# Optimization experiments

Measured on AMD Instinct MI355X. Metric: run time of the kernel, lower is better.

## Reference

```python
import jax, jax.numpy as jnp
import numpy as np

R = 40000      # aug_num_rels
E = 500000     # number of relation-graph triplets
DIN = 64       # rel_emb_dim
DH = 64        # hid_dim_rel
H = 8          # num_head
DHID = DH // H # 8
NBIN = 10
L = 2          # num_layer_rel


def _leaky(x):
    return jax.nn.leaky_relu(x, negative_slope=0.2)


def _rel_layer(emb_rel, head, tail, binidx, pw, pb, abin, avec, aw, ab):
    # emb_rel: [R, DH]; head/tail/binidx: [E]
    concat = jnp.concatenate([emb_rel[head], emb_rel[tail]], axis=-1)  # [E, 2*DH]
    z = _leaky(concat @ pw + pb).reshape(-1, H, DHID)                   # [E, H, DHID]
    # attention logits: per-head dot with attn_vec + leaky(bin bias)
    raw = (z * avec[None]).sum(-1) + _leaky(abin[binidx, :, 0])         # [E, H]
    # segmented softmax over edges grouped by head index
    m = jax.ops.segment_max(raw, head, num_segments=R)                  # [R, H]
    e = jnp.exp(raw - m[head])                                          # [E, H]
    s = jax.ops.segment_sum(e, head, num_segments=R)                    # [R, H]
    beta = e / (s[head] + 1e-16)                                        # [E, H]
    msg = (emb_rel[tail] @ aw + ab).reshape(-1, H, DHID) * beta[..., None]
    out = jax.ops.segment_sum(msg, head, num_segments=R)                # [R, H, DHID]
    return out.reshape(R, DH)


def setup_inputs() -> dict:
    key = jax.random.key(0)
    ks = jax.random.split(key, 12)
    ht = jax.random.randint(ks[0], (E, 2), 0, R)
    b = jax.random.randint(ks[1], (E, 1), 0, NBIN)
    relation_triplets = jnp.concatenate([ht, b], axis=-1).astype(jnp.int64)
    sc = 0.05
    return {
        "relation_triplets": relation_triplets,
        "rel_emb_w": jax.random.normal(ks[2], (R, DIN), jnp.float32) * sc,
        "proj1_w": jax.random.normal(ks[3], (DIN, DH), jnp.float32) * sc,
        "proj1_b": jnp.zeros((DH,), jnp.float32),
        "attn_proj_w": jax.random.normal(ks[4], (L, 2 * DH, DH), jnp.float32) * sc,
        "attn_proj_b": jnp.zeros((L, DH), jnp.float32),
        "attn_bin": jax.random.normal(ks[5], (L, NBIN, H, 1), jnp.float32) * sc,
        "attn_vec": jax.random.normal(ks[6], (L, H, DHID), jnp.float32) * sc,
        "aggr_w": jax.random.normal(ks[7], (L, DH, DH), jnp.float32) * sc,
        "aggr_b": jnp.zeros((L, DH), jnp.float32),
        "res_w": jax.random.normal(ks[8], (L, DH, DH), jnp.float32) * sc,
        "res_b": jnp.zeros((L, DH), jnp.float32),
    }


def reference(relation_triplets, rel_emb_w, proj1_w, proj1_b, attn_proj_w,
              attn_proj_b, attn_bin, attn_vec, aggr_w, aggr_b, res_w, res_b):
    head = relation_triplets[:, 0]
    tail = relation_triplets[:, 1]
    binidx = relation_triplets[:, 2]
    emb_rel = jax.nn.relu(rel_emb_w @ proj1_w + proj1_b)  # [R, DH]
    for l in range(L):
        h = _rel_layer(emb_rel, head, tail, binidx,
                       attn_proj_w[l], attn_proj_b[l], attn_bin[l],
                       attn_vec[l], aggr_w[l], aggr_b[l])
        h = jax.nn.relu(h)
        emb_rel = h + jax.nn.relu(emb_rel @ res_w[l] + res_b[l])
    return emb_rel
```

## Files before the change

kernel.cpp:

```cpp
#include <hip/hip_runtime.h>
#include <hip/hip_bf16.h>

typedef __hip_bfloat16 bf16;

#define R_NUM 40000
#define E_NUM 500000

#define W_P1W 0
#define W_P1B 4096
#define W_APW 4160
#define W_APB 20544
#define W_ABIN 20672
#define W_AVEC 20832
#define W_AW 20960
#define W_AB 29152
#define W_RW 29280
#define W_RB 37472
#define W_END 37600
#define WCONV_BLOCKS 147

#define O_FLAG 0
#define O_WBUF 256
#define O_ROWP 150784
#define O_CNTS 310784
#define O_TMP 470784
#define O_PART 634624
#define O_STB 635136
#define O_BIG 2635392
#define XMP_BYTES 10240000ull
#define HR_BYTES 20480000ull
#define XM32_BYTES 20480000ull
#define NEED_LEAN (O_BIG + XMP_BYTES + HR_BYTES)
#define NEED_XM1 (O_BIG + XM32_BYTES)

static __device__ __forceinline__ float b2f(bf16 x) { return __bfloat162float(x); }
static __device__ __forceinline__ float ldv(const float* p, size_t i) { return p[i]; }
static __device__ __forceinline__ float ldv(const bf16* p, size_t i) { return __bfloat162float(p[i]); }
static __device__ __forceinline__ void stv(float* p, size_t i, float v) { p[i] = v; }
static __device__ __forceinline__ void stv(bf16* p, size_t i, float v) { p[i] = __float2bfloat16(v); }

static __device__ __forceinline__ unsigned int f2bb(float x) {
  union { float f; unsigned int u; } v;
  v.f = x;
  unsigned int r = v.u + 0x7FFFu + ((v.u >> 16) & 1u);
  return r >> 16;
}
static __device__ __forceinline__ unsigned int packxm(float xt, float mt) {
  return f2bb(xt) | (f2bb(mt) << 16);
}


__global__ void k_detect_init(const unsigned int* __restrict__ trip_w,
                              const unsigned short* __restrict__ emb_w, int* __restrict__ flag,
                              int* __restrict__ counts, int* __restrict__ stb) {
  int tid = threadIdx.x;
  if (blockIdx.x == 0) {
    if (tid < 64) {
      int lane = tid;
      unsigned int acc = 0;
      for (int i = lane; i < 1024; i += 64) acc |= trip_w[2 * i + 1];
      int votes = 0;
      for (int i = lane; i < 2048; i += 64) {
        unsigned short u = emb_w[2 * i];
        int ex = (u >> 7) & 0xFF;
        if (ex >= 90 && ex <= 130) votes++;
      }
      for (int off = 1; off < 64; off <<= 1) {
        acc |= __shfl_xor(acc, off);
        votes += __shfl_xor(votes, off);
      }
      if (lane == 0) {
        flag[0] = (acc == 0) ? 1 : 0;
        flag[1] = (votes < 1024) ? 1 : 0;
      }
    }
    return;
  }
  int g = (blockIdx.x - 1) * 256 + tid;
  for (int i = g; i < R_NUM; i += 159 * 256) counts[i] = 0;
  if (blockIdx.x == 1 && tid < 64) stb[E_NUM + tid] = 0;
}


static __device__ __forceinline__ void load_edge(const unsigned int* __restrict__ w, int e,
                                                 int i64, int& h, int& t, int& b) {
  if (i64) {
    h = (int)w[6 * e + 0];
    t = (int)w[6 * e + 2];
    b = (int)w[6 * e + 4];
  } else {
    h = (int)w[3 * e + 0];
    t = (int)w[3 * e + 1];
    b = (int)w[3 * e + 2];
  }
}

__global__ void k_hist_wconv(const unsigned int* __restrict__ trip_w, const int* __restrict__ flag,
                             int* __restrict__ counts, const void* p1w, const void* p1b,
                             const void* apw, const void* apb, const void* abin, const void* avec,
                             const void* aw, const void* ab, const void* rw, const void* rb,
                             float* __restrict__ wbuf) {
  if (blockIdx.x < WCONV_BLOCKS) {
    int i = blockIdx.x * 256 + threadIdx.x;
    if (i >= W_END) return;
    const void* src;
    int off;
    if (i < W_P1B) { src = p1w; off = i - W_P1W; }
    else if (i < W_APW) { src = p1b; off = i - W_P1B; }
    else if (i < W_APB) { src = apw; off = i - W_APW; }
    else if (i < W_ABIN) { src = apb; off = i - W_APB; }
    else if (i < W_AVEC) { src = abin; off = i - W_ABIN; }
    else if (i < W_AW) { src = avec; off = i - W_AVEC; }
    else if (i < W_AB) { src = aw; off = i - W_AW; }
    else if (i < W_RW) { src = ab; off = i - W_AB; }
    else if (i < W_RB) { src = rw; off = i - W_RW; }
    else { src = rb; off = i - W_RB; }
    wbuf[i] = flag[1] ? ((const float*)src)[off] : b2f(((const bf16*)src)[off]);
    return;
  }
  int e = (blockIdx.x - WCONV_BLOCKS) * 256 + threadIdx.x;
  if (e >= E_NUM) return;
  int h, t, b;
  load_edge(trip_w, e, flag[0], h, t, b);
  atomicAdd(&counts[h], 1);
}


__global__ void k_scan_a(const int* __restrict__ counts, int* __restrict__ tmp,
                         int* __restrict__ partial) {
  __shared__ int sd[1024];
  int tid = threadIdx.x;
  int idx = blockIdx.x * 1024 + tid;
  int v = (idx < R_NUM) ? counts[idx] : 0;
  sd[tid] = v;
  __syncthreads();
  for (int off = 1; off < 1024; off <<= 1) {
    int t = (tid >= off) ? sd[tid - off] : 0;
    __syncthreads();
    sd[tid] += t;
    __syncthreads();
  }
  if (idx < R_NUM) tmp[idx] = sd[tid];
  if (tid == 1023) partial[blockIdx.x] = sd[1023];
}

__global__ void k_scan_c(const int* __restrict__ counts, const int* __restrict__ tmp,
                         const int* __restrict__ partial, int* __restrict__ row_ptr) {
  __shared__ int soff;
  if (threadIdx.x < 64) {
    int lane = threadIdx.x;
    int p = (lane < (int)blockIdx.x) ? partial[lane] : 0;
    for (int d = 1; d < 64; d <<= 1) p += __shfl_xor(p, d);
    if (lane == 0) soff = p;
  }
  __syncthreads();
  int idx = blockIdx.x * 1024 + threadIdx.x;
  if (idx < R_NUM) row_ptr[idx] = tmp[idx] - counts[idx] + soff;
}

__global__ void k_scatter(const unsigned int* __restrict__ trip_w, const int* __restrict__ flag,
                          int* __restrict__ row_ptr, int* __restrict__ stb) {
  int e = blockIdx.x * 256 + threadIdx.x;
  if (e >= E_NUM) return;
  int h, t, b;
  load_edge(trip_w, e, flag[0], h, t, b);
  int pos = atomicAdd(&row_ptr[h], 1);
  stb[pos] = (t & 0xFFFF) | (b << 16);
}


__global__ void __launch_bounds__(256, 4) k_emb0xm_p(const void* __restrict__ A,
                                                     const int* __restrict__ flag,
                                                     const float* __restrict__ wbuf,
                                                     float* __restrict__ emb,
                                                     unsigned int* __restrict__ XMp,
                                                     float2* __restrict__ HR) {
  int j = threadIdx.x & 63;
  int g = threadIdx.x >> 6;
  int r0 = blockIdx.x * 32 + g * 8;
  int f32 = flag[1];
  __shared__ float sA[32][64];
  for (int k = threadIdx.x; k < 2048; k += 256) {
    int rr = k >> 6, cc = k & 63;
    size_t idx = (size_t)(blockIdx.x * 32 + rr) * 64 + cc;
    sA[rr][cc] = f32 ? ((const float*)A)[idx] : b2f(((const bf16*)A)[idx]);
  }
  __syncthreads();
  int base = g * 8;
  float a[8] = {0.f, 0.f, 0.f, 0.f, 0.f, 0.f, 0.f, 0.f};
  {
    const float* W = wbuf + W_P1W;
    for (int i4 = 0; i4 < 64; i4 += 4) {
      float4 ev[8];
#pragma unroll
      for (int n = 0; n < 8; n++) ev[n] = *(const float4*)&sA[base + n][i4];
#pragma unroll
      for (int di = 0; di < 4; di++) {
        float w = W[(i4 + di) * 64 + j];
#pragma unroll
        for (int n = 0; n < 8; n++)
          a[n] = fmaf(((const float*)&ev[n])[di], w, a[n]);
      }
    }
    float bj = wbuf[W_P1B + j];
#pragma unroll
    for (int n = 0; n < 8; n++) {
      a[n] = fmaxf(a[n] + bj, 0.f);
      emb[(size_t)(r0 + n) * 64 + j] = a[n];
    }
  }
  __syncthreads();
#pragma unroll
  for (int n = 0; n < 8; n++) sA[base + n][j] = a[n];
  __syncthreads();
  {
    const float* pwb = wbuf + W_APW + 4096;
    const float* aw = wbuf + W_AW;
    const float* pwt = wbuf + W_APW;
    const float* rw = wbuf + W_RW;
    float axt[8] = {0.f, 0.f, 0.f, 0.f, 0.f, 0.f, 0.f, 0.f};
    float amt[8] = {0.f, 0.f, 0.f, 0.f, 0.f, 0.f, 0.f, 0.f};
    float axh[8] = {0.f, 0.f, 0.f, 0.f, 0.f, 0.f, 0.f, 0.f};
    float ars[8] = {0.f, 0.f, 0.f, 0.f, 0.f, 0.f, 0.f, 0.f};
    for (int i4 = 0; i4 < 64; i4 += 4) {
      float4 ev[8];
#pragma unroll
      for (int n = 0; n < 8; n++) ev[n] = *(const float4*)&sA[base + n][i4];
#pragma unroll
      for (int di = 0; di < 4; di++) {
        int i = i4 + di;
        float wt = pwb[i * 64 + j];
        float wm = aw[i * 64 + j];
        float wh = pwt[i * 64 + j];
        float wr = rw[i * 64 + j];
#pragma unroll
        for (int n = 0; n < 8; n++) {
          float e = ((const float*)&ev[n])[di];
          axt[n] = fmaf(e, wt, axt[n]);
          amt[n] = fmaf(e, wm, amt[n]);
          axh[n] = fmaf(e, wh, axh[n]);
          ars[n] = fmaf(e, wr, ars[n]);
        }
      }
    }
    float abj = wbuf[W_AB + j];
    float pbj = wbuf[W_APB + j];
    float rbj = wbuf[W_RB + j];
#pragma unroll
    for (int n = 0; n < 8; n++) {
      XMp[(size_t)(r0 + n) * 64 + j] = packxm(axt[n], amt[n] + abj);
      HR[(size_t)(r0 + n) * 64 + j] = make_float2(axh[n] + pbj, fmaxf(ars[n] + rbj, 0.f));
    }
  }
}


__global__ void __launch_bounds__(256, 4) k_xmhr_p(const float* __restrict__ emb,
                                                   const float* __restrict__ wbuf, int l,
                                                   unsigned int* __restrict__ XMp,
                                                   float2* __restrict__ HR) {
  int j = threadIdx.x & 63;
  int g = threadIdx.x >> 6;
  int r0 = blockIdx.x * 32 + g * 8;
  __shared__ float sE[32][64];
  for (int k = threadIdx.x; k < 2048; k += 256) {
    int rr = k >> 6, cc = k & 63;
    sE[rr][cc] = emb[(size_t)(blockIdx.x * 32 + rr) * 64 + cc];
  }
  __syncthreads();
  int base = g * 8;
  const float* pwb = wbuf + W_APW + l * 8192 + 4096;
  const float* aw = wbuf + W_AW + l * 4096;
  const float* pwt = wbuf + W_APW + l * 8192;
  const float* rw = wbuf + W_RW + l * 4096;
  float axt[8] = {0.f, 0.f, 0.f, 0.f, 0.f, 0.f, 0.f, 0.f};
  float amt[8] = {0.f, 0.f, 0.f, 0.f, 0.f, 0.f, 0.f, 0.f};
  float axh[8] = {0.f, 0.f, 0.f, 0.f, 0.f, 0.f, 0.f, 0.f};
  float ars[8] = {0.f, 0.f, 0.f, 0.f, 0.f, 0.f, 0.f, 0.f};
  for (int i4 = 0; i4 < 64; i4 += 4) {
    float4 ev[8];
#pragma unroll
    for (int n = 0; n < 8; n++) ev[n] = *(const float4*)&sE[base + n][i4];
#pragma unroll
    for (int di = 0; di < 4; di++) {
      int i = i4 + di;
      float wt = pwb[i * 64 + j];
      float wm = aw[i * 64 + j];
      float wh = pwt[i * 64 + j];
      float wr = rw[i * 64 + j];
#pragma unroll
      for (int n = 0; n < 8; n++) {
        float e = ((const float*)&ev[n])[di];
        axt[n] = fmaf(e, wt, axt[n]);
        amt[n] = fmaf(e, wm, amt[n]);
        axh[n] = fmaf(e, wh, axh[n]);
        ars[n] = fmaf(e, wr, ars[n]);
      }
    }
  }
  float abj = wbuf[W_AB + l * 64 + j];
  float pbj = wbuf[W_APB + l * 64 + j];
  float rbj = wbuf[W_RB + l * 64 + j];
#pragma unroll
  for (int n = 0; n < 8; n++) {
    XMp[(size_t)(r0 + n) * 64 + j] = packxm(axt[n], amt[n] + abj);
    HR[(size_t)(r0 + n) * 64 + j] = make_float2(axh[n] + pbj, fmaxf(ars[n] + rbj, 0.f));
  }
}


__global__ void __launch_bounds__(256, 4) k_edge_lean(
    const int* __restrict__ row_ptr, const int* __restrict__ stb,
    const unsigned int* __restrict__ XMp, const float2* __restrict__ HR,
    const float* __restrict__ wbuf, int l, float* __restrict__ emb) {
  __shared__ float sab[80];
  int tid = threadIdx.x;
  int lane = tid & 63;
  int w = tid >> 6;
  int hh = lane >> 3;
  if (tid < 80) {
    float a = wbuf[W_ABIN + l * 80 + tid];
    sab[tid] = (a > 0.f) ? a : 0.2f * a;
  }
  __syncthreads();
  float av = wbuf[W_AVEC + l * 64 + lane];

  int r = blockIdx.x * 4 + w;
  float2 hr = HR[(size_t)r * 64 + lane];
  int beg = (r == 0) ? 0 : row_ptr[r - 1];
  int end = row_ptr[r];
  beg = __builtin_amdgcn_readfirstlane(beg);
  end = __builtin_amdgcn_readfirstlane(end);

  float xh = hr.x;
  float num = 0.f, den = 0.f;
  for (int j = beg; j < end; j += 16) {
    int pk[16];
    unsigned int xp[16];
#pragma unroll
    for (int k = 0; k < 16; k++) pk[k] = stb[j + k];
#pragma unroll
    for (int k = 0; k < 16; k++)
      xp[k] = XMp[(size_t)(pk[k] & 0xFFFF) * 64 + lane];
#pragma unroll
    for (int k = 0; k < 16; k++) {
      float xt = __uint_as_float(xp[k] << 16);
      float mt = __uint_as_float(xp[k] & 0xFFFF0000u);
      float z = xh + xt;
      z = (z > 0.f) ? z : 0.2f * z;
      float v = z * av;
      v += __shfl_xor(v, 1);
      v += __shfl_xor(v, 2);
      v += __shfl_xor(v, 4);
      float e = __expf(v + sab[(pk[k] >> 16) * 8 + hh]);
      e = (j + k < end) ? e : 0.f;
      den += e;
      num = fmaf(mt, e, num);
    }
  }
  emb[(size_t)r * 64 + lane] = fmaxf(num / (den + 1e-16f), 0.f) + hr.y;
}


__global__ void k_emb0(const void* __restrict__ A, const int* __restrict__ flag,
                       const float* __restrict__ wbuf, float* __restrict__ emb) {
  int j = threadIdx.x & 63;
  int g = threadIdx.x >> 6;
  int r0 = blockIdx.x * 16 + g * 4;
  int f32 = flag[1];
  __shared__ float sA[16][64];
  for (int k = threadIdx.x; k < 1024; k += 256) {
    int rr = k >> 6, cc = k & 63;
    size_t idx = (size_t)(blockIdx.x * 16 + rr) * 64 + cc;
    sA[rr][cc] = f32 ? ((const float*)A)[idx] : b2f(((const bf16*)A)[idx]);
  }
  __syncthreads();
  const float* W = wbuf + W_P1W;
  float a[4] = {0.f, 0.f, 0.f, 0.f};
  int base = g * 4;
  for (int i = 0; i < 64; i++) {
    float w = W[i * 64 + j];
#pragma unroll
    for (int n = 0; n < 4; n++) a[n] = fmaf(sA[base + n][i], w, a[n]);
  }
  float bj = wbuf[W_P1B + j];
#pragma unroll
  for (int n = 0; n < 4; n++)
    emb[(size_t)(r0 + n) * 64 + j] = fmaxf(a[n] + bj, 0.f);
}

__global__ void k_xm(const float* __restrict__ emb, const float* __restrict__ wbuf, int l,
                     float2* __restrict__ XM) {
  int j = threadIdx.x & 63;
  int g = threadIdx.x >> 6;
  int r0 = blockIdx.x * 16 + g * 4;
  __shared__ float sE[16][64];
  for (int k = threadIdx.x; k < 1024; k += 256) {
    int rr = k >> 6, cc = k & 63;
    sE[rr][cc] = emb[(size_t)(blockIdx.x * 16 + rr) * 64 + cc];
  }
  __syncthreads();
  const float* pwb = wbuf + W_APW + l * 8192 + 4096;
  const float* aw = wbuf + W_AW + l * 4096;
  float axt[4] = {0.f, 0.f, 0.f, 0.f};
  float amt[4] = {0.f, 0.f, 0.f, 0.f};
  int base = g * 4;
  for (int i = 0; i < 64; i++) {
    float wt = pwb[i * 64 + j];
    float wm = aw[i * 64 + j];
#pragma unroll
    for (int n = 0; n < 4; n++) {
      float e = sE[base + n][i];
      axt[n] = fmaf(e, wt, axt[n]);
      amt[n] = fmaf(e, wm, amt[n]);
    }
  }
  float abj = wbuf[W_AB + l * 64 + j];
#pragma unroll
  for (int n = 0; n < 4; n++)
    XM[(size_t)(r0 + n) * 64 + j] = make_float2(axt[n], amt[n] + abj);
}

__global__ void __launch_bounds__(256, 4) k_edge_f(
    const int* __restrict__ row_ptr, const int* __restrict__ stb, const float2* __restrict__ XM,
    const float* __restrict__ wbuf, int l, float* __restrict__ emb) {
  __shared__ float sab[80];
  int tid = threadIdx.x;
  int lane = tid & 63;
  int w = tid >> 6;
  int hh = lane >> 3;
  if (tid < 80) {
    float a = wbuf[W_ABIN + l * 80 + tid];
    sab[tid] = (a > 0.f) ? a : 0.2f * a;
  }
  __syncthreads();

  const float* pwt = wbuf + W_APW + l * 8192;
  const float* rwp = wbuf + W_RW + l * 4096;
  float av = wbuf[W_AVEC + l * 64 + lane];
  float xh0 = wbuf[W_APB + l * 64 + lane];
  float res0 = wbuf[W_RB + l * 64 + lane];

  int r0 = blockIdx.x * 16 + w * 4;
  for (int rr = 0; rr < 4; rr++) {
    int r = r0 + rr;
    float ev = emb[(size_t)r * 64 + lane];
    float xh = xh0, res = res0;
#pragma unroll 16
    for (int i = 0; i < 64; i++) {
      float e = __shfl(ev, i);
      xh = fmaf(e, pwt[i * 64 + lane], xh);
      res = fmaf(e, rwp[i * 64 + lane], res);
    }
    res = fmaxf(res, 0.f);

    int beg = (r == 0) ? 0 : row_ptr[r - 1];
    int end = row_ptr[r];
    beg = __builtin_amdgcn_readfirstlane(beg);
    end = __builtin_amdgcn_readfirstlane(end);

    float num = 0.f, den = 0.f;
    for (int j = beg; j < end; j += 16) {
      int pk[16];
      float2 xmv[16];
#pragma unroll
      for (int k = 0; k < 16; k++) pk[k] = stb[j + k];
#pragma unroll
      for (int k = 0; k < 16; k++) xmv[k] = XM[(size_t)(pk[k] & 0xFFFF) * 64 + lane];
#pragma unroll
      for (int k = 0; k < 16; k++) {
        float z = xh + xmv[k].x;
        z = (z > 0.f) ? z : 0.2f * z;
        float v = z * av;
        v += __shfl_xor(v, 1);
        v += __shfl_xor(v, 2);
        v += __shfl_xor(v, 4);
        float e = __expf(v + sab[(pk[k] >> 16) * 8 + hh]);
        e = (j + k < end) ? e : 0.f;
        den += e;
        num = fmaf(xmv[k].y, e, num);
      }
    }
    emb[(size_t)r * 64 + lane] = fmaxf(num / (den + 1e-16f), 0.f) + res;
  }
}


static __device__ __forceinline__ float dotcol(const float* __restrict__ Wm, float val, int lane) {
  float acc = 0.f;
  for (int i = 0; i < 64; i++) acc = fmaf(__shfl(val, i), Wm[i * 64 + lane], acc);
  return acc;
}

template <typename TIN, typename TOUT>
__global__ void k_edge_d(const int* __restrict__ row_ptr, const int* __restrict__ stb,
                         const float* __restrict__ wbuf, int l, const TIN* __restrict__ emb_in,
                         TOUT* __restrict__ emb_out) {
  __shared__ float sab[80];
  int tid = threadIdx.x;
  int lane = tid & 63;
  int w = tid >> 6;
  int r = blockIdx.x * 4 + w;
  int hh = lane >> 3;
  if (tid < 80) {
    float a = wbuf[W_ABIN + l * 80 + tid];
    sab[tid] = (a > 0.f) ? a : 0.2f * a;
  }
  __syncthreads();
  const float* pwt = wbuf + W_APW + l * 8192;
  const float* pwb = pwt + 4096;
  const float* aw = wbuf + W_AW + l * 4096;
  const float* rw = wbuf + W_RW + l * 4096;

  float ev = ldv(emb_in, (size_t)r * 64 + lane);
  float xh = wbuf[W_APB + l * 64 + lane];
  float res = wbuf[W_RB + l * 64 + lane];
  for (int i = 0; i < 64; i++) {
    float e = __shfl(ev, i);
    xh = fmaf(e, pwt[i * 64 + lane], xh);
    res = fmaf(e, rw[i * 64 + lane], res);
  }
  res = fmaxf(res, 0.f);
  float av = wbuf[W_AVEC + l * 64 + lane];
  float abl = wbuf[W_AB + l * 64 + lane];

  int beg = (r == 0) ? 0 : row_ptr[r - 1];
  int end = row_ptr[r];
  float num = 0.f, den = 0.f;
  for (int j = beg; j < end; j++) {
    int p = stb[j];
    int t = p & 0xFFFF;
    float tv = ldv(emb_in, (size_t)t * 64 + lane);
    float z = xh + dotcol(pwb, tv, lane);
    z = (z > 0.f) ? z : 0.2f * z;
    float v = z * av;
    v += __shfl_xor(v, 1);
    v += __shfl_xor(v, 2);
    v += __shfl_xor(v, 4);
    float e = __expf(v + sab[(p >> 16) * 8 + hh]);
    den += e;
    float mt = dotcol(aw, tv, lane) + abl;
    num = fmaf(mt, e, num);
  }
  stv(emb_out, (size_t)r * 64 + lane, fmaxf(num / (den + 1e-16f), 0.f) + res);
}


extern "C" void kernel_launch(void* const* d_in, const int* in_sizes, int n_in,
                              void* d_out, int out_size, void* d_ws, size_t ws_size,
                              hipStream_t stream) {
  const unsigned int* trip_w = (const unsigned int*)d_in[0];
  const void* rel_emb = d_in[1];
  float* emb = (float*)d_out;

  char* ws = (char*)d_ws;
  int* flag = (int*)(ws + O_FLAG);
  float* wbuf = (float*)(ws + O_WBUF);
  int* row_ptr = (int*)(ws + O_ROWP);
  int* counts = (int*)(ws + O_CNTS);
  int* tmp = (int*)(ws + O_TMP);
  int* partial = (int*)(ws + O_PART);
  int* stb = (int*)(ws + O_STB);
  char* big = ws + O_BIG;

  k_detect_init<<<160, 256, 0, stream>>>(trip_w, (const unsigned short*)rel_emb, flag, counts,
                                         stb);
  int eb_blocks = (E_NUM + 255) / 256;
  k_hist_wconv<<<WCONV_BLOCKS + eb_blocks, 256, 0, stream>>>(
      trip_w, flag, counts, d_in[2], d_in[3], d_in[4], d_in[5], d_in[6], d_in[7], d_in[8],
      d_in[9], d_in[10], d_in[11], wbuf);
  k_scan_a<<<40, 1024, 0, stream>>>(counts, tmp, partial);
  k_scan_c<<<40, 1024, 0, stream>>>(counts, tmp, partial, row_ptr);
  k_scatter<<<eb_blocks, 256, 0, stream>>>(trip_w, flag, row_ptr, stb);

  if (ws_size >= NEED_LEAN) {
    unsigned int* XMp = (unsigned int*)big;
    float2* HR = (float2*)(big + XMP_BYTES);
    k_emb0xm_p<<<R_NUM / 32, 256, 0, stream>>>(rel_emb, flag, wbuf, emb, XMp, HR);
    k_edge_lean<<<R_NUM / 4, 256, 0, stream>>>(row_ptr, stb, XMp, HR, wbuf, 0, emb);
    k_xmhr_p<<<R_NUM / 32, 256, 0, stream>>>(emb, wbuf, 1, XMp, HR);
    k_edge_lean<<<R_NUM / 4, 256, 0, stream>>>(row_ptr, stb, XMp, HR, wbuf, 1, emb);
  } else if (ws_size >= NEED_XM1) {
    float2* XM = (float2*)big;
    k_emb0<<<R_NUM / 16, 256, 0, stream>>>(rel_emb, flag, wbuf, emb);
    k_xm<<<R_NUM / 16, 256, 0, stream>>>(emb, wbuf, 0, XM);
    k_edge_f<<<R_NUM / 16, 256, 0, stream>>>(row_ptr, stb, XM, wbuf, 0, emb);
    k_xm<<<R_NUM / 16, 256, 0, stream>>>(emb, wbuf, 1, XM);
    k_edge_f<<<R_NUM / 16, 256, 0, stream>>>(row_ptr, stb, XM, wbuf, 1, emb);
  } else {
    k_emb0<<<R_NUM / 16, 256, 0, stream>>>(rel_emb, flag, wbuf, emb);
    bf16* embB = (bf16*)big;
    k_edge_d<float, bf16><<<R_NUM / 4, 256, 0, stream>>>(row_ptr, stb, wbuf, 0, emb, embB);
    k_edge_d<bf16, float><<<R_NUM / 4, 256, 0, stream>>>(row_ptr, stb, wbuf, 1, embB, emb);
  }
}
```

Baseline: 259.7 us.

## Fuse scan passes, merge scatter with embedding kernel, process two rows per wave

```diff
diff --git a/kernel.cpp b/kernel.cpp
--- a/kernel.cpp
+++ b/kernel.cpp
@@ -18,15 +18,16 @@
 #define W_RB 37472
 #define W_END 37600
 #define WCONV_BLOCKS 147
+#define SCAT_BLOCKS 1954
+#define EMB_BLOCKS 1250
 
 #define O_FLAG 0
 #define O_WBUF 256
 #define O_ROWP 150784
 #define O_CNTS 310784
-#define O_TMP 470784
-#define O_PART 634624
-#define O_STB 635136
-#define O_BIG 2635392
+#define O_PART 470784
+#define O_STB 471040
+#define O_BIG 2471296
 #define XMP_BYTES 10240000ull
 #define HR_BYTES 20480000ull
 #define XM32_BYTES 20480000ull
@@ -52,7 +53,8 @@
 
 __global__ void k_detect_init(const unsigned int* __restrict__ trip_w,
                               const unsigned short* __restrict__ emb_w, int* __restrict__ flag,
-                              int* __restrict__ counts, int* __restrict__ stb) {
+                              int* __restrict__ counts, int* __restrict__ stb,
+                              int* __restrict__ partial) {
   int tid = threadIdx.x;
   if (blockIdx.x == 0) {
     if (tid < 64) {
@@ -78,7 +80,10 @@
   }
   int g = (blockIdx.x - 1) * 256 + tid;
   for (int i = g; i < R_NUM; i += 159 * 256) counts[i] = 0;
-  if (blockIdx.x == 1 && tid < 64) stb[E_NUM + tid] = 0;
+  if (blockIdx.x == 1 && tid < 64) {
+    stb[E_NUM + tid] = 0;
+    partial[tid] = -1;
+  }
 }
 
 
@@ -126,11 +131,13 @@
 }
 
 
-__global__ void k_scan_a(const int* __restrict__ counts, int* __restrict__ tmp,
-                         int* __restrict__ partial) {
+__global__ void k_scan1(const int* __restrict__ counts, int* __restrict__ partial,
+                        int* __restrict__ row_ptr) {
   __shared__ int sd[1024];
+  __shared__ int soff;
   int tid = threadIdx.x;
-  int idx = blockIdx.x * 1024 + tid;
+  int b = blockIdx.x;
+  int idx = b * 1024 + tid;
   int v = (idx < R_NUM) ? counts[idx] : 0;
   sd[tid] = v;
   __syncthreads();
@@ -140,49 +147,44 @@
     sd[tid] += t;
     __syncthreads();
   }
-  if (idx < R_NUM) tmp[idx] = sd[tid];
-  if (tid == 1023) partial[blockIdx.x] = sd[1023];
-}
-
-__global__ void k_scan_c(const int* __restrict__ counts, const int* __restrict__ tmp,
-                         const int* __restrict__ partial, int* __restrict__ row_ptr) {
-  __shared__ int soff;
-  if (threadIdx.x < 64) {
-    int lane = threadIdx.x;
-    int p = (lane < (int)blockIdx.x) ? partial[lane] : 0;
-    for (int d = 1; d < 64; d <<= 1) p += __shfl_xor(p, d);
-    if (lane == 0) soff = p;
-  }
-  __syncthreads();
-  int idx = blockIdx.x * 1024 + threadIdx.x;
-  if (idx < R_NUM) row_ptr[idx] = tmp[idx] - counts[idx] + soff;
-}
-
-__global__ void k_scatter(const unsigned int* __restrict__ trip_w, const int* __restrict__ flag,
-                          int* __restrict__ row_ptr, int* __restrict__ stb) {
-  int e = blockIdx.x * 256 + threadIdx.x;
-  if (e >= E_NUM) return;
-  int h, t, b;
-  load_edge(trip_w, e, flag[0], h, t, b);
-  int pos = atomicAdd(&row_ptr[h], 1);
-  stb[pos] = (t & 0xFFFF) | (b << 16);
-}
-
-
-__global__ void __launch_bounds__(256, 4) k_emb0xm_p(const void* __restrict__ A,
-                                                     const int* __restrict__ flag,
-                                                     const float* __restrict__ wbuf,
-                                                     float* __restrict__ emb,
-                                                     unsigned int* __restrict__ XMp,
-                                                     float2* __restrict__ HR) {
+  if (tid == 0) {
+    atomicExch(&partial[b], sd[1023]);
+    int s = 0;
+    for (int i = 0; i < b; i++) {
+      int p;
+      do { p = atomicAdd(&partial[i], 0); } while (p == -1);
+      s += p;
+    }
+    soff = s;
+  }
+  __syncthreads();
+  if (idx < R_NUM) row_ptr[idx] = soff + sd[tid] - v;
+}
+
+
+__global__ void __launch_bounds__(256, 4) k_scat_emb(
+    const unsigned int* __restrict__ trip_w, const int* __restrict__ flag,
+    int* __restrict__ row_ptr, int* __restrict__ stb, const void* __restrict__ A,
+    const float* __restrict__ wbuf, float* __restrict__ emb, unsigned int* __restrict__ XMp,
+    float2* __restrict__ HR) {
+  if (blockIdx.x < SCAT_BLOCKS) {
+    int e = blockIdx.x * 256 + threadIdx.x;
+    if (e >= E_NUM) return;
+    int h, t, b;
+    load_edge(trip_w, e, flag[0], h, t, b);
+    int pos = atomicAdd(&row_ptr[h], 1);
+    stb[pos] = (t & 0xFFFF) | (b << 16);
+    return;
+  }
+  int bid = blockIdx.x - SCAT_BLOCKS;
   int j = threadIdx.x & 63;
   int g = threadIdx.x >> 6;
-  int r0 = blockIdx.x * 32 + g * 8;
+  int r0 = bid * 32 + g * 8;
   int f32 = flag[1];
   __shared__ float sA[32][64];
   for (int k = threadIdx.x; k < 2048; k += 256) {
     int rr = k >> 6, cc = k & 63;
-    size_t idx = (size_t)(blockIdx.x * 32 + rr) * 64 + cc;
+    size_t idx = (size_t)(bid * 32 + rr) * 64 + cc;
     sA[rr][cc] = f32 ? ((const float*)A)[idx] : b2f(((const bf16*)A)[idx]);
   }
   __syncthreads();
@@ -308,6 +310,39 @@
   }
 }
 
+
+static __device__ __forceinline__ void consume16(const int* pk, const unsigned int* xp, float xh,
+                                                 float av, const float* sab, int hh, int j0,
+                                                 int end, float& num, float& den) {
+#pragma unroll
+  for (int k = 0; k < 16; k++) {
+    float xt = __uint_as_float(xp[k] << 16);
+    float mt = __uint_as_float(xp[k] & 0xFFFF0000u);
+    float z = xh + xt;
+    z = (z > 0.f) ? z : 0.2f * z;
+    float v = z * av;
+    v += __shfl_xor(v, 1);
+    v += __shfl_xor(v, 2);
+    v += __shfl_xor(v, 4);
+    float e = __expf(v + sab[(pk[k] >> 16) * 8 + hh]);
+    e = (j0 + k < end) ? e : 0.f;
+    den += e;
+    num = fmaf(mt, e, num);
+  }
+}
+
+static __device__ __forceinline__ void edge_window(const int* __restrict__ stb,
+                                                   const unsigned int* __restrict__ XMp, int j,
+                                                   int end, int lane, int hh, float xh, float av,
+                                                   const float* sab, float& num, float& den) {
+  int pk[16];
+  unsigned int xp[16];
+#pragma unroll
+  for (int k = 0; k < 16; k++) pk[k] = stb[j + k];
+#pragma unroll
+  for (int k = 0; k < 16; k++) xp[k] = XMp[(size_t)(pk[k] & 0xFFFF) * 64 + lane];
+  consume16(pk, xp, xh, av, sab, hh, j, end, num, den);
+}
 
 __global__ void __launch_bounds__(256, 4) k_edge_lean(
     const int* __restrict__ row_ptr, const int* __restrict__ stb,
@@ -325,42 +360,51 @@
   __syncthreads();
   float av = wbuf[W_AVEC + l * 64 + lane];
 
-  int r = blockIdx.x * 4 + w;
-  float2 hr = HR[(size_t)r * 64 + lane];
-  int beg = (r == 0) ? 0 : row_ptr[r - 1];
-  int end = row_ptr[r];
-  beg = __builtin_amdgcn_readfirstlane(beg);
-  end = __builtin_amdgcn_readfirstlane(end);
-
-  float xh = hr.x;
-  float num = 0.f, den = 0.f;
-  for (int j = beg; j < end; j += 16) {
-    int pk[16];
-    unsigned int xp[16];
-#pragma unroll
-    for (int k = 0; k < 16; k++) pk[k] = stb[j + k];
-#pragma unroll
-    for (int k = 0; k < 16; k++)
-      xp[k] = XMp[(size_t)(pk[k] & 0xFFFF) * 64 + lane];
-#pragma unroll
-    for (int k = 0; k < 16; k++) {
-      float xt = __uint_as_float(xp[k] << 16);
-      float mt = __uint_as_float(xp[k] & 0xFFFF0000u);
-      float z = xh + xt;
-      z = (z > 0.f) ? z : 0.2f * z;
-      float v = z * av;
-      v += __shfl_xor(v, 1);
-      v += __shfl_xor(v, 2);
-      v += __shfl_xor(v, 4);
-      float e = __expf(v + sab[(pk[k] >> 16) * 8 + hh]);
-      e = (j + k < end) ? e : 0.f;
-      den += e;
-      num = fmaf(mt, e, num);
-    }
-  }
-  emb[(size_t)r * 64 + lane] = fmaxf(num / (den + 1e-16f), 0.f) + hr.y;
-}
-
+  int r = blockIdx.x * 8 + w * 2;
+  float2 hrA = HR[(size_t)r * 64 + lane];
+  float2 hrB = HR[(size_t)(r + 1) * 64 + lane];
+  int begA = (r == 0) ? 0 : row_ptr[r - 1];
+  int endA = row_ptr[r];
+  int endB = row_ptr[r + 1];
+  begA = __builtin_amdgcn_readfirstlane(begA);
+  endA = __builtin_amdgcn_readfirstlane(endA);
+  endB = __builtin_amdgcn_readfirstlane(endB);
+  int begB = endA;
+
+  float numA = 0.f, denA = 0.f, numB = 0.f, denB = 0.f;
+  {
+    int pkA[16], pkB[16];
+    unsigned int xpA[16], xpB[16];
+#pragma unroll
+    for (int k = 0; k < 16; k++) pkA[k] = stb[begA + k];
+#pragma unroll
+    for (int k = 0; k < 16; k++) pkB[k] = stb[begB + k];
+#pragma unroll
+    for (int k = 0; k < 16; k++) xpA[k] = XMp[(size_t)(pkA[k] & 0xFFFF) * 64 + lane];
+#pragma unroll
+    for (int k = 0; k < 16; k++) xpB[k] = XMp[(size_t)(pkB[k] & 0xFFFF) * 64 + lane];
+    consume16(pkA, xpA, hrA.x, av, sab, hh, begA, endA, numA, denA);
+    consume16(pkB, xpB, hrB.x, av, sab, hh, begB, endB, numB, denB);
+  }
+  for (int j = begA + 16; j < endA; j += 16)
+    edge_window(stb, XMp, j, endA, lane, hh, hrA.x, av, sab, numA, denA);
+  for (int j = begB + 16; j < endB; j += 16)
+    edge_window(stb, XMp, j, endB, lane, hh, hrB.x, av, sab, numB, denB);
+
+  emb[(size_t)r * 64 + lane] = fmaxf(numA / (denA + 1e-16f), 0.f) + hrA.y;
+  emb[(size_t)(r + 1) * 64 + lane] = fmaxf(numB / (denB + 1e-16f), 0.f) + hrB.y;
+}
+
+
+__global__ void k_scatter(const unsigned int* __restrict__ trip_w, const int* __restrict__ flag,
+                          int* __restrict__ row_ptr, int* __restrict__ stb) {
+  int e = blockIdx.x * 256 + threadIdx.x;
+  if (e >= E_NUM) return;
+  int h, t, b;
+  load_edge(trip_w, e, flag[0], h, t, b);
+  int pos = atomicAdd(&row_ptr[h], 1);
+  stb[pos] = (t & 0xFFFF) | (b << 16);
+}
 
 __global__ void k_emb0(const void* __restrict__ A, const int* __restrict__ flag,
                        const float* __restrict__ wbuf, float* __restrict__ emb) {
@@ -484,7 +528,6 @@
     emb[(size_t)r * 64 + lane] = fmaxf(num / (den + 1e-16f), 0.f) + res;
   }
 }
-
 
 static __device__ __forceinline__ float dotcol(const float* __restrict__ Wm, float val, int lane) {
   float acc = 0.f;
@@ -558,36 +601,36 @@
   float* wbuf = (float*)(ws + O_WBUF);
   int* row_ptr = (int*)(ws + O_ROWP);
   int* counts = (int*)(ws + O_CNTS);
-  int* tmp = (int*)(ws + O_TMP);
   int* partial = (int*)(ws + O_PART);
   int* stb = (int*)(ws + O_STB);
   char* big = ws + O_BIG;
 
   k_detect_init<<<160, 256, 0, stream>>>(trip_w, (const unsigned short*)rel_emb, flag, counts,
-                                         stb);
+                                         stb, partial);
   int eb_blocks = (E_NUM + 255) / 256;
   k_hist_wconv<<<WCONV_BLOCKS + eb_blocks, 256, 0, stream>>>(
       trip_w, flag, counts, d_in[2], d_in[3], d_in[4], d_in[5], d_in[6], d_in[7], d_in[8],
       d_in[9], d_in[10], d_in[11], wbuf);
-  k_scan_a<<<40, 1024, 0, stream>>>(counts, tmp, partial);
-  k_scan_c<<<40, 1024, 0, stream>>>(counts, tmp, partial, row_ptr);
-  k_scatter<<<eb_blocks, 256, 0, stream>>>(trip_w, flag, row_ptr, stb);
+  k_scan1<<<40, 1024, 0, stream>>>(counts, partial, row_ptr);
 
   if (ws_size >= NEED_LEAN) {
     unsigned int* XMp = (unsigned int*)big;
     float2* HR = (float2*)(big + XMP_BYTES);
-    k_emb0xm_p<<<R_NUM / 32, 256, 0, stream>>>(rel_emb, flag, wbuf, emb, XMp, HR);
-    k_edge_lean<<<R_NUM / 4, 256, 0, stream>>>(row_ptr, stb, XMp, HR, wbuf, 0, emb);
+    k_scat_emb<<<SCAT_BLOCKS + EMB_BLOCKS, 256, 0, stream>>>(trip_w, flag, row_ptr, stb, rel_emb,
+                                                             wbuf, emb, XMp, HR);
+    k_edge_lean<<<R_NUM / 8, 256, 0, stream>>>(row_ptr, stb, XMp, HR, wbuf, 0, emb);
     k_xmhr_p<<<R_NUM / 32, 256, 0, stream>>>(emb, wbuf, 1, XMp, HR);
-    k_edge_lean<<<R_NUM / 4, 256, 0, stream>>>(row_ptr, stb, XMp, HR, wbuf, 1, emb);
+    k_edge_lean<<<R_NUM / 8, 256, 0, stream>>>(row_ptr, stb, XMp, HR, wbuf, 1, emb);
   } else if (ws_size >= NEED_XM1) {
     float2* XM = (float2*)big;
+    k_scatter<<<eb_blocks, 256, 0, stream>>>(trip_w, flag, row_ptr, stb);
     k_emb0<<<R_NUM / 16, 256, 0, stream>>>(rel_emb, flag, wbuf, emb);
     k_xm<<<R_NUM / 16, 256, 0, stream>>>(emb, wbuf, 0, XM);
     k_edge_f<<<R_NUM / 16, 256, 0, stream>>>(row_ptr, stb, XM, wbuf, 0, emb);
     k_xm<<<R_NUM / 16, 256, 0, stream>>>(emb, wbuf, 1, XM);
     k_edge_f<<<R_NUM / 16, 256, 0, stream>>>(row_ptr, stb, XM, wbuf, 1, emb);
   } else {
+    k_scatter<<<eb_blocks, 256, 0, stream>>>(trip_w, flag, row_ptr, stb);
     k_emb0<<<R_NUM / 16, 256, 0, stream>>>(rel_emb, flag, wbuf, emb);
     bf16* embB = (bf16*)big;
     k_edge_d<float, bf16><<<R_NUM / 4, 256, 0, stream>>>(row_ptr, stb, wbuf, 0, emb, embB);
```

Result: slower. 282.6 us (+8.8%).
